# Kernel tuning notes

Measured on AMD Instinct MI355X. Metric: run time of the kernel, lower is better.

Reference implementation:

```python
import jax, jax.numpy as jnp
import numpy as np

N_NODES = 50000


def _sage_conv(x, src, dst, W_l, b_l, W_r):
    # PyG SAGEConv (aggr='mean'): out = lin_l(mean_{j in N(i)} x_j) + lin_r(x_i)
    # lin_l has bias, lin_r has no bias.
    neigh_sum = jax.ops.segment_sum(x[src], dst, num_segments=N_NODES)  # [N, F]
    deg = jax.ops.segment_sum(jnp.ones_like(dst, dtype=x.dtype), dst, num_segments=N_NODES)
    neigh_mean = neigh_sum / jnp.maximum(deg, 1.0)[:, None]
    return neigh_mean @ W_l.T + b_l + x @ W_r.T


def setup_inputs() -> dict:
    key = jax.random.key(0)
    ks = jax.random.split(key, 8)
    D, H, C = 768, 128, 4
    x = jax.random.normal(ks[0], (N_NODES, D), dtype=jnp.float32)
    edge_index = jax.random.randint(ks[1], (2, 800000), 0, N_NODES, dtype=jnp.int64)
    s1 = 1.0 / np.sqrt(D)
    s2 = 1.0 / np.sqrt(H)
    return {
        "x": x,
        "edge_index": edge_index,
        "W1_l": jax.random.uniform(ks[2], (H, D), jnp.float32, -s1, s1),
        "b1_l": jnp.zeros((H,), jnp.float32),
        "W1_r": jax.random.uniform(ks[3], (H, D), jnp.float32, -s1, s1),
        "W2_l": jax.random.uniform(ks[4], (C, H), jnp.float32, -s2, s2),
        "b2_l": jnp.zeros((C,), jnp.float32),
        "W2_r": jax.random.uniform(ks[5], (C, H), jnp.float32, -s2, s2),
    }


def reference(x, edge_index, W1_l, b1_l, W1_r, W2_l, b2_l, W2_r):
    src, dst = edge_index[0], edge_index[1]
    h = jax.nn.relu(_sage_conv(x, src, dst, W1_l, b1_l, W1_r))  # [N, H]
    out = _sage_conv(h, src, dst, W2_l, b2_l, W2_r)  # [N, C]
    return out
```

## Files before the change

### kernel.cpp

```cpp
#include <hip/hip_runtime.h>


typedef __bf16 bf16x8 __attribute__((ext_vector_type(8)));
typedef float  f32x4  __attribute__((ext_vector_type(4)));

__device__ __forceinline__ float bf16_lo(uint32_t w) {
    union { uint32_t u; float f; } c; c.u = w << 16; return c.f;
}
__device__ __forceinline__ float bf16_hi(uint32_t w) {
    union { uint32_t u; float f; } c; c.u = w & 0xffff0000u; return c.f;
}

__global__ __launch_bounds__(256)
void prep(const float* __restrict__ W1l, const float* __restrict__ W1r,
          __bf16* __restrict__ Bp, int* __restrict__ deg, int N)
{
    int i = blockIdx.x * 256 + threadIdx.x;
    if (i < N) deg[i] = 0;
    if (i < 256 * 768) {
        int col = i / 768, k = i - col * 768;
        float v = (col < 128) ? W1l[col * 768 + k] : W1r[(col - 128) * 768 + k];
        Bp[((k >> 3) << 11) + (col << 3) + (k & 7)] = (__bf16)v;
    }
}

__global__ __launch_bounds__(256)
void csr_count(const int* __restrict__ ei, int* __restrict__ deg, int E)
{
    int e = blockIdx.x * 256 + threadIdx.x;
    if (e >= E) return;
    atomicAdd(&deg[ei[E + e]], 1);
}

__global__ __launch_bounds__(1024)
void scan1(const int* __restrict__ deg, int* __restrict__ row_ptr,
           int* __restrict__ partials, int N)
{
    __shared__ int buf[1024];
    int i = blockIdx.x * 1024 + threadIdx.x;
    int v = (i < N) ? deg[i] : 0;
    int val = v;
    buf[threadIdx.x] = val;
    __syncthreads();
    for (int off = 1; off < 1024; off <<= 1) {
        int t = (threadIdx.x >= (unsigned)off) ? buf[threadIdx.x - off] : 0;
        __syncthreads();
        val += t;
        buf[threadIdx.x] = val;
        __syncthreads();
    }
    if (i < N) row_ptr[i] = val - v;
    if (threadIdx.x == 1023) partials[blockIdx.x] = val;
}

__global__ __launch_bounds__(1024)
void scan23(int* __restrict__ row_ptr, int* __restrict__ cursor,
            const int* __restrict__ partials, int N, int E, int nb)
{
    __shared__ int soff;
    int b = blockIdx.x;
    if (threadIdx.x < 64) {
        int lane = threadIdx.x;
        int v = (lane < nb) ? partials[lane] : 0;
        int s = v;
        #pragma unroll
        for (int off = 1; off < 64; off <<= 1) {
            int t = __shfl_up(s, off);
            if (lane >= off) s += t;
        }
        if (lane == b) soff = s - v;
    }
    __syncthreads();
    int off = soff;
    int i = b * 1024 + threadIdx.x;
    if (i < N) {
        int v = row_ptr[i] + off;
        row_ptr[i] = v;
        cursor[i]  = v;
    }
    if (b == 0 && threadIdx.x == 0) row_ptr[N] = E;
}

__global__ __launch_bounds__(256)
void gemm_fill(const float* __restrict__ x, const __bf16* __restrict__ Bp,
               __bf16* __restrict__ Cb, int M, int mtiles,
               const int* __restrict__ ei, int* __restrict__ cursor,
               int* __restrict__ csr_src, int E)
{
    __shared__ __bf16 As[2][32][72];
    const int tid = threadIdx.x;

    if ((int)blockIdx.x >= mtiles) {
        int stride = (gridDim.x - mtiles) * 256;
        for (int e = (blockIdx.x - mtiles) * 256 + tid; e < E; e += stride) {
            int src = ei[e];
            int dst = ei[E + e];
            int pos = atomicAdd(&cursor[dst], 1);
            csr_src[pos] = src;
        }
        return;
    }

    const int bm   = blockIdx.x * 32;
    const int lane = tid & 63;
    const int wc   = tid >> 6;
    const int l15  = lane & 15;
    const int lk   = lane >> 4;

    f32x4 acc[2][4] = {};

    const int srow = tid >> 3;
    const int scol = (tid & 7) << 3;
    const float* gsrc = x + (size_t)min(bm + srow, M - 1) * 768 + scol;

    const __bf16* bbase = Bp + ((size_t)(wc * 64 + l15) << 3) + ((size_t)lk << 11);

    float4 ap0, ap1;
    auto load_A = [&](int k0) {
        ap0 = *(const float4*)(gsrc + k0);
        ap1 = *(const float4*)(gsrc + k0 + 4);
    };

    load_A(0);
    for (int kt = 0; kt < 12; ++kt) {
        const int buf = kt & 1;
        {
            bf16x8 b;
            b[0] = (__bf16)ap0.x; b[1] = (__bf16)ap0.y;
            b[2] = (__bf16)ap0.z; b[3] = (__bf16)ap0.w;
            b[4] = (__bf16)ap1.x; b[5] = (__bf16)ap1.y;
            b[6] = (__bf16)ap1.z; b[7] = (__bf16)ap1.w;
            *(bf16x8*)&As[buf][srow][scol] = b;
        }
        __syncthreads();
        if (kt < 11) load_A((kt + 1) * 64);

        #pragma unroll
        for (int ks = 0; ks < 2; ++ks) {
            bf16x8 bcur[4];
            #pragma unroll
            for (int j = 0; j < 4; ++j)
                bcur[j] = *(const bf16x8*)(bbase +
                    (((size_t)(kt * 8 + ks * 4) << 11) + ((size_t)j << 7)));
            bf16x8 af[2];
            #pragma unroll
            for (int i = 0; i < 2; ++i)
                af[i] = *(const bf16x8*)&As[buf][i * 16 + l15][ks * 32 + lk * 8];
            #pragma unroll
            for (int i = 0; i < 2; ++i)
                #pragma unroll
                for (int j = 0; j < 4; ++j)
                    acc[i][j] = __builtin_amdgcn_mfma_f32_16x16x32_bf16(
                        af[i], bcur[j], acc[i][j], 0, 0, 0);
        }
    }

    #pragma unroll
    for (int i = 0; i < 2; ++i)
        #pragma unroll
        for (int j = 0; j < 4; ++j)
            #pragma unroll
            for (int v = 0; v < 4; ++v) {
                int row = bm + i * 16 + lk * 4 + v;
                int col = wc * 64 + j * 16 + l15;
                if (row < M) Cb[(size_t)row * 256 + col] = (__bf16)acc[i][j][v];
            }
}

__global__ __launch_bounds__(256)
void sage1_fused(const int* __restrict__ row_ptr, const int* __restrict__ csr_src,
                 const __bf16* __restrict__ pq, const float* __restrict__ b1,
                 const float* __restrict__ W2l, const float* __restrict__ W2r,
                 float* __restrict__ r, float* __restrict__ s, int N)
{
    __shared__ float Wl[512], Wr[512];
    for (int i = threadIdx.x; i < 512; i += 256) {
        Wl[i] = W2l[i];
        Wr[i] = W2r[i];
    }
    __syncthreads();

    int wid  = threadIdx.x >> 6;
    int lane = threadIdx.x & 63;
    int g = lane >> 3;
    int l = lane & 7;
    int n = blockIdx.x * 4 + wid;
    if (n >= N) return;
    int beg = row_ptr[n], end = row_ptr[n + 1];

    float a0[8] = {}, a1[8] = {};
    for (int eb = beg; eb < end; eb += 64) {
        int cnt = min(64, end - eb);
        int id = (eb + lane < end) ? csr_src[eb + lane] : 0;
        for (int t = 0; t < cnt; t += 8) {
            int src = __shfl(id, t + g);
            if (t + g < cnt) {
                const __bf16* row = pq + (size_t)src * 256;
                uint4 w0 = *(const uint4*)(row + l * 8);
                uint4 w1 = *(const uint4*)(row + 64 + l * 8);
                a0[0] += bf16_lo(w0.x); a0[1] += bf16_hi(w0.x);
                a0[2] += bf16_lo(w0.y); a0[3] += bf16_hi(w0.y);
                a0[4] += bf16_lo(w0.z); a0[5] += bf16_hi(w0.z);
                a0[6] += bf16_lo(w0.w); a0[7] += bf16_hi(w0.w);
                a1[0] += bf16_lo(w1.x); a1[1] += bf16_hi(w1.x);
                a1[2] += bf16_lo(w1.y); a1[3] += bf16_hi(w1.y);
                a1[4] += bf16_lo(w1.z); a1[5] += bf16_hi(w1.z);
                a1[6] += bf16_lo(w1.w); a1[7] += bf16_hi(w1.w);
            }
        }
    }
    #pragma unroll
    for (int c = 0; c < 8; ++c) {
        a0[c] += __shfl_xor(a0[c], 8);  a1[c] += __shfl_xor(a1[c], 8);
        a0[c] += __shfl_xor(a0[c], 16); a1[c] += __shfl_xor(a1[c], 16);
        a0[c] += __shfl_xor(a0[c], 32); a1[c] += __shfl_xor(a1[c], 32);
    }

    float inv = 1.0f / fmaxf((float)(end - beg), 1.0f);
    const __bf16* qrow = pq + (size_t)n * 256 + 128;
    uint4  qw0 = *(const uint4*)(qrow + l * 8);
    uint4  qw1 = *(const uint4*)(qrow + 64 + l * 8);
    float4 bv00 = *(const float4*)(b1 + l * 8);
    float4 bv01 = *(const float4*)(b1 + l * 8 + 4);
    float4 bv10 = *(const float4*)(b1 + 64 + l * 8);
    float4 bv11 = *(const float4*)(b1 + 64 + l * 8 + 4);
    float h0[8], h1[8];
    h0[0] = fmaxf(a0[0] * inv + bv00.x + bf16_lo(qw0.x), 0.f);
    h0[1] = fmaxf(a0[1] * inv + bv00.y + bf16_hi(qw0.x), 0.f);
    h0[2] = fmaxf(a0[2] * inv + bv00.z + bf16_lo(qw0.y), 0.f);
    h0[3] = fmaxf(a0[3] * inv + bv00.w + bf16_hi(qw0.y), 0.f);
    h0[4] = fmaxf(a0[4] * inv + bv01.x + bf16_lo(qw0.z), 0.f);
    h0[5] = fmaxf(a0[5] * inv + bv01.y + bf16_hi(qw0.z), 0.f);
    h0[6] = fmaxf(a0[6] * inv + bv01.z + bf16_lo(qw0.w), 0.f);
    h0[7] = fmaxf(a0[7] * inv + bv01.w + bf16_hi(qw0.w), 0.f);
    h1[0] = fmaxf(a1[0] * inv + bv10.x + bf16_lo(qw1.x), 0.f);
    h1[1] = fmaxf(a1[1] * inv + bv10.y + bf16_hi(qw1.x), 0.f);
    h1[2] = fmaxf(a1[2] * inv + bv10.z + bf16_lo(qw1.y), 0.f);
    h1[3] = fmaxf(a1[3] * inv + bv10.w + bf16_hi(qw1.y), 0.f);
    h1[4] = fmaxf(a1[4] * inv + bv11.x + bf16_lo(qw1.z), 0.f);
    h1[5] = fmaxf(a1[5] * inv + bv11.y + bf16_hi(qw1.z), 0.f);
    h1[6] = fmaxf(a1[6] * inv + bv11.z + bf16_lo(qw1.w), 0.f);
    h1[7] = fmaxf(a1[7] * inv + bv11.w + bf16_hi(qw1.w), 0.f);

    float part[8];
    #pragma unroll
    for (int c = 0; c < 4; ++c) {
        float pl = 0.f, pr = 0.f;
        #pragma unroll
        for (int j = 0; j < 8; ++j) {
            pl = fmaf(h0[j], Wl[c * 128 + l * 8 + j], pl);
            pl = fmaf(h1[j], Wl[c * 128 + 64 + l * 8 + j], pl);
            pr = fmaf(h0[j], Wr[c * 128 + l * 8 + j], pr);
            pr = fmaf(h1[j], Wr[c * 128 + 64 + l * 8 + j], pr);
        }
        part[c] = pl; part[4 + c] = pr;
    }
    #pragma unroll
    for (int off = 4; off; off >>= 1)
        #pragma unroll
        for (int c = 0; c < 8; ++c)
            part[c] += __shfl_xor(part[c], off);
    if (lane == 0) {
        *(float4*)(r + (size_t)n * 4) = make_float4(part[0], part[1], part[2], part[3]);
        *(float4*)(s + (size_t)n * 4) = make_float4(part[4], part[5], part[6], part[7]);
    }
}

__global__ __launch_bounds__(256)
void sage2_gather(const int* __restrict__ row_ptr, const int* __restrict__ csr_src,
                  const float* __restrict__ r, const float* __restrict__ s,
                  const float* __restrict__ b2, float* __restrict__ out, int N)
{
    int t = blockIdx.x * 256 + threadIdx.x;
    if (t >= N * 4) return;
    int n = t >> 2, c = t & 3;
    int beg = row_ptr[n], end = row_ptr[n + 1];
    float acc = 0.f;
    for (int e = beg; e < end; ++e)
        acc += r[(size_t)csr_src[e] * 4 + c];
    out[t] = acc / fmaxf((float)(end - beg), 1.0f) + b2[c] + s[t];
}

extern "C" void kernel_launch(void* const* d_in, const int* in_sizes, int n_in,
                              void* d_out, int out_size, void* d_ws, size_t ws_size,
                              hipStream_t stream)
{
    const float* x   = (const float*)d_in[0];
    const int*   ei  = (const int*)d_in[1];
    const float* W1l = (const float*)d_in[2];
    const float* b1l = (const float*)d_in[3];
    const float* W1r = (const float*)d_in[4];
    const float* W2l = (const float*)d_in[5];
    const float* b2l = (const float*)d_in[6];
    const float* W2r = (const float*)d_in[7];
    float* out = (float*)d_out;

    const int N = in_sizes[0] / 768;
    const int E = in_sizes[1] / 2;
    const int NB = (N + 1023) / 1024;
    const int mtiles = (N + 31) / 32;

    char* ws = (char*)d_ws;
    size_t off = 0;
    auto alloc = [&](size_t bytes) -> void* {
        void* pp = ws + off;
        off += (bytes + 255) & ~(size_t)255;
        return pp;
    };
    __bf16* pq      = (__bf16*)alloc((size_t)N * 256 * 2);
    float*  r       = (float*)alloc((size_t)N * 4 * 4);
    float*  s       = (float*)alloc((size_t)N * 4 * 4);
    __bf16* Bp      = (__bf16*)alloc((size_t)256 * 768 * 2);
    int*    deg     = (int*)alloc((size_t)N * 4);
    int*    row_ptr = (int*)alloc((size_t)(N + 1) * 4);
    int*    cursor  = (int*)alloc((size_t)N * 4);
    int*    csr_src = (int*)alloc((size_t)E * 4);
    int*    partials= (int*)alloc((size_t)64 * 4);

    prep<<<(256 * 768 + 255) / 256, 256, 0, stream>>>(W1l, W1r, Bp, deg, N);

    csr_count<<<(E + 255) / 256, 256, 0, stream>>>(ei, deg, E);
    scan1<<<NB, 1024, 0, stream>>>(deg, row_ptr, partials, N);
    scan23<<<NB, 1024, 0, stream>>>(row_ptr, cursor, partials, N, E, NB);

    gemm_fill<<<mtiles + 256, 256, 0, stream>>>(x, Bp, pq, N, mtiles,
                                                ei, cursor, csr_src, E);

    sage1_fused<<<(N + 3) / 4, 256, 0, stream>>>(row_ptr, csr_src, pq, b1l,
                                                 W2l, W2r, r, s, N);

    sage2_gather<<<(N * 4 + 255) / 256, 256, 0, stream>>>(row_ptr, csr_src, r, s, b2l, out, N);
}
```

Measured before the change: 202.9 us.

## Retile layer-1 GEMM to 64x64 tiles with shared-memory B and XCD-aware job mapping

The layer-1 GEMM changes from 32-row tiles covering all 256 output columns, with B read directly from a pre-swizzled global layout, to 64x64 output tiles. Both A and B are now staged through shared memory, and block IDs are remapped so that consecutive jobs land on the same XCD for L2 locality. The weight prep kernel now writes a plain row-major bf16 matrix. Each x row is now read by four blocks instead of one, which raises global/L2 traffic on the dominant fp32 input. The double-buffered LDS is also replaced by single buffering with an extra barrier per iteration.

```diff
diff --git a/kernel.cpp b/kernel.cpp
--- a/kernel.cpp
+++ b/kernel.cpp
@@ -13,14 +13,14 @@
 
 __global__ __launch_bounds__(256)
 void prep(const float* __restrict__ W1l, const float* __restrict__ W1r,
-          __bf16* __restrict__ Bp, int* __restrict__ deg, int N)
+          __bf16* __restrict__ Wb, int* __restrict__ deg, int N)
 {
     int i = blockIdx.x * 256 + threadIdx.x;
     if (i < N) deg[i] = 0;
     if (i < 256 * 768) {
-        int col = i / 768, k = i - col * 768;
-        float v = (col < 128) ? W1l[col * 768 + k] : W1r[(col - 128) * 768 + k];
-        Bp[((k >> 3) << 11) + (col << 3) + (k & 7)] = (__bf16)v;
+        int n = i / 768, k = i - n * 768;
+        float v = (n < 128) ? W1l[n * 768 + k] : W1r[(n - 128) * 768 + k];
+        Wb[i] = (__bf16)v;
     }
 }
 
@@ -82,17 +82,19 @@
 }
 
 __global__ __launch_bounds__(256)
-void gemm_fill(const float* __restrict__ x, const __bf16* __restrict__ Bp,
-               __bf16* __restrict__ Cb, int M, int mtiles,
+void gemm_fill(const float* __restrict__ A, const __bf16* __restrict__ Bw,
+               __bf16* __restrict__ Cb, int M, int gblocks,
                const int* __restrict__ ei, int* __restrict__ cursor,
                int* __restrict__ csr_src, int E)
 {
-    __shared__ __bf16 As[2][32][72];
+    constexpr int LDK = 72;
+    __shared__ __bf16 As[64][LDK];
+    __shared__ __bf16 Bs[64][LDK];
     const int tid = threadIdx.x;
 
-    if ((int)blockIdx.x >= mtiles) {
-        int stride = (gridDim.x - mtiles) * 256;
-        for (int e = (blockIdx.x - mtiles) * 256 + tid; e < E; e += stride) {
+    if ((int)blockIdx.x >= gblocks) {
+        int stride = (gridDim.x - gblocks) * 256;
+        for (int e = (blockIdx.x - gblocks) * 256 + tid; e < E; e += stride) {
             int src = ei[e];
             int dst = ei[E + e];
             int pos = atomicAdd(&cursor[dst], 1);
@@ -101,68 +103,87 @@
         return;
     }
 
-    const int bm   = blockIdx.x * 32;
+    const int p   = blockIdx.x;
+    const int xcd = p & 7, kk = p >> 3;
+    const int q   = gblocks >> 3, rem = gblocks & 7;
+    const int base = (xcd < rem) ? xcd * (q + 1) : rem * (q + 1) + (xcd - rem) * q;
+    const int job = base + kk;
+    const int bm  = (job >> 2) * 64;
+    const int bn  = (job & 3) * 64;
+
     const int lane = tid & 63;
-    const int wc   = tid >> 6;
-    const int l15  = lane & 15;
-    const int lk   = lane >> 4;
-
-    f32x4 acc[2][4] = {};
-
-    const int srow = tid >> 3;
-    const int scol = (tid & 7) << 3;
-    const float* gsrc = x + (size_t)min(bm + srow, M - 1) * 768 + scol;
-
-    const __bf16* bbase = Bp + ((size_t)(wc * 64 + l15) << 3) + ((size_t)lk << 11);
-
-    float4 ap0, ap1;
-    auto load_A = [&](int k0) {
-        ap0 = *(const float4*)(gsrc + k0);
-        ap1 = *(const float4*)(gsrc + k0 + 4);
+    const int wave = tid >> 6;
+    const int wr = wave >> 1, wc = wave & 1;
+    const int l15 = lane & 15;
+    const int lk  = lane >> 4;
+
+    f32x4 acc[2][2] = {};
+    float4 apref[2][2];
+    bf16x8 bpref[2];
+
+    auto load_tile = [&](int k0) {
+        #pragma unroll
+        for (int it = 0; it < 2; ++it) {
+            int v = it * 256 + tid;
+            int row = v >> 3, kc = (v & 7) << 3;
+            if (bm + row < M) {
+                const float* src = A + (size_t)(bm + row) * 768 + k0 + kc;
+                apref[it][0] = *(const float4*)src;
+                apref[it][1] = *(const float4*)(src + 4);
+            } else {
+                apref[it][0] = make_float4(0.f, 0.f, 0.f, 0.f);
+                apref[it][1] = make_float4(0.f, 0.f, 0.f, 0.f);
+            }
+            bpref[it] = *(const bf16x8*)(Bw + (size_t)(bn + row) * 768 + k0 + kc);
+        }
     };
 
-    load_A(0);
+    load_tile(0);
     for (int kt = 0; kt < 12; ++kt) {
-        const int buf = kt & 1;
-        {
+        if (kt) __syncthreads();
+        #pragma unroll
+        for (int it = 0; it < 2; ++it) {
+            int v = it * 256 + tid;
+            int row = v >> 3, kc = (v & 7) << 3;
+            float4 f0 = apref[it][0], f1 = apref[it][1];
             bf16x8 b;
-            b[0] = (__bf16)ap0.x; b[1] = (__bf16)ap0.y;
-            b[2] = (__bf16)ap0.z; b[3] = (__bf16)ap0.w;
-            b[4] = (__bf16)ap1.x; b[5] = (__bf16)ap1.y;
-            b[6] = (__bf16)ap1.z; b[7] = (__bf16)ap1.w;
-            *(bf16x8*)&As[buf][srow][scol] = b;
+            b[0] = (__bf16)f0.x; b[1] = (__bf16)f0.y;
+            b[2] = (__bf16)f0.z; b[3] = (__bf16)f0.w;
+            b[4] = (__bf16)f1.x; b[5] = (__bf16)f1.y;
+            b[6] = (__bf16)f1.z; b[7] = (__bf16)f1.w;
+            *(bf16x8*)&As[row][kc] = b;
+            *(bf16x8*)&Bs[row][kc] = bpref[it];
         }
         __syncthreads();
-        if (kt < 11) load_A((kt + 1) * 64);
+        if (kt < 11) load_tile((kt + 1) * 64);
 
         #pragma unroll
         for (int ks = 0; ks < 2; ++ks) {
-            bf16x8 bcur[4];
-            #pragma unroll
-            for (int j = 0; j < 4; ++j)
-                bcur[j] = *(const bf16x8*)(bbase +
-                    (((size_t)(kt * 8 + ks * 4) << 11) + ((size_t)j << 7)));
-            bf16x8 af[2];
+            int koff = ks * 32 + lk * 8;
+            bf16x8 af[2], bfr[2];
             #pragma unroll
             for (int i = 0; i < 2; ++i)
-                af[i] = *(const bf16x8*)&As[buf][i * 16 + l15][ks * 32 + lk * 8];
+                af[i] = *(const bf16x8*)&As[wr * 32 + i * 16 + l15][koff];
+            #pragma unroll
+            for (int j = 0; j < 2; ++j)
+                bfr[j] = *(const bf16x8*)&Bs[wc * 32 + j * 16 + l15][koff];
             #pragma unroll
             for (int i = 0; i < 2; ++i)
                 #pragma unroll
-                for (int j = 0; j < 4; ++j)
+                for (int j = 0; j < 2; ++j)
                     acc[i][j] = __builtin_amdgcn_mfma_f32_16x16x32_bf16(
-                        af[i], bcur[j], acc[i][j], 0, 0, 0);
+                        af[i], bfr[j], acc[i][j], 0, 0, 0);
         }
     }
 
     #pragma unroll
     for (int i = 0; i < 2; ++i)
         #pragma unroll
-        for (int j = 0; j < 4; ++j)
+        for (int j = 0; j < 2; ++j)
             #pragma unroll
             for (int v = 0; v < 4; ++v) {
-                int row = bm + i * 16 + lk * 4 + v;
-                int col = wc * 64 + j * 16 + l15;
+                int row = bm + wr * 32 + i * 16 + lk * 4 + v;
+                int col = bn + wc * 32 + j * 16 + l15;
                 if (row < M) Cb[(size_t)row * 256 + col] = (__bf16)acc[i][j][v];
             }
 }
@@ -298,7 +319,8 @@
     const int N = in_sizes[0] / 768;
     const int E = in_sizes[1] / 2;
     const int NB = (N + 1023) / 1024;
-    const int mtiles = (N + 31) / 32;
+    const int mtiles  = (N + 63) / 64;
+    const int gblocks = mtiles * 4;
 
     char* ws = (char*)d_ws;
     size_t off = 0;
@@ -310,21 +332,21 @@
     __bf16* pq      = (__bf16*)alloc((size_t)N * 256 * 2);
     float*  r       = (float*)alloc((size_t)N * 4 * 4);
     float*  s       = (float*)alloc((size_t)N * 4 * 4);
-    __bf16* Bp      = (__bf16*)alloc((size_t)256 * 768 * 2);
+    __bf16* Wb      = (__bf16*)alloc((size_t)256 * 768 * 2);
     int*    deg     = (int*)alloc((size_t)N * 4);
     int*    row_ptr = (int*)alloc((size_t)(N + 1) * 4);
     int*    cursor  = (int*)alloc((size_t)N * 4);
     int*    csr_src = (int*)alloc((size_t)E * 4);
     int*    partials= (int*)alloc((size_t)64 * 4);
 
-    prep<<<(256 * 768 + 255) / 256, 256, 0, stream>>>(W1l, W1r, Bp, deg, N);
+    prep<<<(256 * 768 + 255) / 256, 256, 0, stream>>>(W1l, W1r, Wb, deg, N);
 
     csr_count<<<(E + 255) / 256, 256, 0, stream>>>(ei, deg, E);
     scan1<<<NB, 1024, 0, stream>>>(deg, row_ptr, partials, N);
     scan23<<<NB, 1024, 0, stream>>>(row_ptr, cursor, partials, N, E, NB);
 
-    gemm_fill<<<mtiles + 256, 256, 0, stream>>>(x, Bp, pq, N, mtiles,
-                                                ei, cursor, csr_src, E);
+    gemm_fill<<<gblocks + 256, 256, 0, stream>>>(x, Wb, pq, N, gblocks,
+                                                 ei, cursor, csr_src, E);
 
     sage1_fused<<<(N + 3) / 4, 256, 0, stream>>>(row_ptr, csr_src, pq, b1l,
                                                  W2l, W2r, r, s, N);
```

Measured after the change: 204.4 us. No clear change (+0.7%).
